# Kernel tuning notes

Measured on AMD Instinct MI355X. Metric: run time of the kernel, lower is better.

The kernel has to match this reference:

```python
import jax, jax.numpy as jnp
import numpy as np

TEMP = 0.05
MOMENTUM = 0.2
EPS = 1e-12

B, D, N = 64, 256, 200000


def setup_inputs() -> dict:
    key = jax.random.key(0)
    k1, k2, k3, k4 = jax.random.split(key, 4)
    inputs = jax.random.normal(k1, (B, D), dtype=jnp.float32)
    scores = jax.random.uniform(k2, (B,), dtype=jnp.float32)
    features = jax.random.normal(k3, (N, D), dtype=jnp.float32)
    # memory bank rows are kept L2-normalized by the update rule
    features = features / jnp.linalg.norm(features, axis=1, keepdims=True)
    targets = jax.random.randint(k4, (B,), 0, N, dtype=jnp.int64)
    return {"inputs": inputs, "scores": scores, "features": features, "targets": targets}


def reference(inputs, scores, features, targets):
    # L2-normalize query features (F.normalize(inputs, dim=1))
    x = inputs / jnp.maximum(jnp.linalg.norm(inputs, axis=1, keepdims=True), EPS)
    # memory-bank lookup: [B, N] logits against the full bank
    logits = jnp.einsum("bd,nd->bn", x, features) / TEMP
    logp = jax.nn.log_softmax(logits, axis=-1)
    per_sample_ce = -jnp.take_along_axis(logp, targets[:, None], axis=1)[:, 0]
    loss = jnp.sum(scores * per_sample_ce)
    # momentum scatter-update of the indexed bank rows with per-row renorm
    old = features[targets]                                   # [B, D] gather
    upd = MOMENTUM * old + (1.0 - MOMENTUM) * scores[:, None] * x
    upd = upd / jnp.maximum(jnp.linalg.norm(upd, axis=1, keepdims=True), EPS)
    new_features = features.at[targets].set(upd)
    return loss, new_features
```

## Files before the change

kernel.cpp:

```cpp
#include <hip/hip_runtime.h>
#include <hip/hip_bf16.h>

#define BB      64
#define DD      256
#define NROWS   200000
#define TEMP_INV 20.0f
#define MOM     0.2f
#define OMOM    0.8f
#define EPSN    1e-12f

#define TILE_R  16
#define NTILES  (NROWS / TILE_R)
#define GRID_B  1024

__device__ __forceinline__ float wave_allreduce_sum(float v) {
#pragma unroll
    for (int m = 32; m >= 1; m >>= 1) v += __shfl_xor(v, m, 64);
    return v;
}

__global__ void normalize_kernel(const float* __restrict__ inputs,
                                 float* __restrict__ xq,
                                 float* __restrict__ gsum,
                                 float* __restrict__ out) {
    int b = blockIdx.x, l = threadIdx.x;
    const float4* in4 = (const float4*)inputs;
    float4 v = in4[b * 64 + l];
    float ss = v.x * v.x + v.y * v.y + v.z * v.z + v.w * v.w;
    ss = wave_allreduce_sum(ss);
    float inv = 1.0f / fmaxf(sqrtf(ss), EPSN);
    float4 x = make_float4(v.x * inv, v.y * inv, v.z * inv, v.w * inv);
    ((float4*)xq)[l * 64 + b] = x;
    if (l == 0) gsum[b] = 0.0f;
    if (b == 0 && l == 0) out[0] = 0.0f;
}

__global__ __launch_bounds__(256, 3) void bank_kernel(
    const float* __restrict__ feat,
    const float* __restrict__ xq,
    float* __restrict__ out,
    float* __restrict__ gsum) {
    __shared__ float4 fld[TILE_R * 64];
    __shared__ float  part[4][TILE_R][BB];
    __shared__ float  fin[4][BB];

    int tid = threadIdx.x;
    int w = tid >> 6, l = tid & 63;

    const float4* xq4 = (const float4*)xq;
    float4 xr[16];
#pragma unroll
    for (int j = 0; j < 16; ++j) xr[j] = xq4[(w * 16 + j) * 64 + l];

    const float4* feat4 = (const float4*)feat;
    float* outF = out + 1;
    const float* fldF = (const float*)fld;
    float psum = 0.0f;

    for (int tile = blockIdx.x; tile < NTILES; tile += (int)gridDim.x) {
        int base4 = tile * (TILE_R * 64);
        float4 v0 = feat4[base4 + tid];
        float4 v1 = feat4[base4 + tid + 256];
        float4 v2 = feat4[base4 + tid + 512];
        float4 v3 = feat4[base4 + tid + 768];
        fld[tid]       = v0;
        fld[tid + 256] = v1;
        fld[tid + 512] = v2;
        fld[tid + 768] = v3;
        __syncthreads();

        int base = tile * (TILE_R * DD);
#pragma unroll
        for (int k = 0; k < 16; ++k)
            outF[base + tid + 256 * k] = fldF[tid + 256 * k];

        float p[TILE_R];
#pragma unroll
        for (int r = 0; r < TILE_R; ++r) p[r] = 0.0f;
#pragma unroll
        for (int j = 0; j < 16; ++j) {
            float4 xj = xr[j];
#pragma unroll
            for (int r = 0; r < TILE_R; ++r) {
                float4 f = fld[r * 64 + w * 16 + j];
                p[r] = fmaf(xj.x, f.x, p[r]);
                p[r] = fmaf(xj.y, f.y, p[r]);
                p[r] = fmaf(xj.z, f.z, p[r]);
                p[r] = fmaf(xj.w, f.w, p[r]);
            }
        }
#pragma unroll
        for (int r = 0; r < TILE_R; ++r) part[w][r][l] = p[r];
        __syncthreads();

#pragma unroll
        for (int i = 0; i < 4; ++i) {
            int r = (w << 2) | i;
            float dsum = part[0][r][l] + part[1][r][l]
                       + part[2][r][l] + part[3][r][l];
            psum += __expf(fmaf(dsum, TEMP_INV, -20.0f));
        }
        __syncthreads();
    }

    fin[w][l] = psum;
    __syncthreads();
    if (tid < BB) {
        float s = fin[0][tid] + fin[1][tid] + fin[2][tid] + fin[3][tid];
        atomicAdd(&gsum[tid], s);
    }
}

__global__ void update_kernel(const float* __restrict__ inputs,
                              const float* __restrict__ scores,
                              const float* __restrict__ feat,
                              const int* __restrict__ targets,
                              const float* __restrict__ gsum,
                              float* __restrict__ out) {
    int b = blockIdx.x, l = threadIdx.x;
    const float4* in4 = (const float4*)inputs;
    float4 v = in4[b * 64 + l];
    float ss = wave_allreduce_sum(v.x * v.x + v.y * v.y + v.z * v.z + v.w * v.w);
    float inv = 1.0f / fmaxf(sqrtf(ss), EPSN);
    float4 x = make_float4(v.x * inv, v.y * inv, v.z * inv, v.w * inv);

    int t = targets[b];
    const float4* feat4 = (const float4*)feat;
    float4 old = feat4[t * 64 + l];

    float dt = wave_allreduce_sum(x.x * old.x + x.y * old.y +
                                  x.z * old.z + x.w * old.w);
    float sc = scores[b];
    float c = OMOM * sc;
    float4 u = make_float4(MOM * old.x + c * x.x,
                           MOM * old.y + c * x.y,
                           MOM * old.z + c * x.z,
                           MOM * old.w + c * x.w);
    float us = wave_allreduce_sum(u.x * u.x + u.y * u.y + u.z * u.z + u.w * u.w);
    float uinv = 1.0f / fmaxf(sqrtf(us), EPSN);
    u.x *= uinv; u.y *= uinv; u.z *= uinv; u.w *= uinv;

    float* outF = out + 1;
    int bi = t * DD + 4 * l;
    outF[bi]     = u.x;
    outF[bi + 1] = u.y;
    outF[bi + 2] = u.z;
    outF[bi + 3] = u.w;

    if (l == 0) {
        float lse = 20.0f + logf(gsum[b]);
        float ce  = lse - dt * TEMP_INV;
        atomicAdd(&out[0], sc * ce);
    }
}

extern "C" void kernel_launch(void* const* d_in, const int* in_sizes, int n_in,
                              void* d_out, int out_size, void* d_ws, size_t ws_size,
                              hipStream_t stream) {
    const float* inputs  = (const float*)d_in[0];
    const float* scores  = (const float*)d_in[1];
    const float* feat    = (const float*)d_in[2];
    const int*   targets = (const int*)d_in[3];
    float* out = (float*)d_out;

    float* xq   = (float*)d_ws;
    float* gsum = xq + 16384;

    normalize_kernel<<<64, 64, 0, stream>>>(inputs, xq, gsum, out);
    bank_kernel<<<GRID_B, 256, 0, stream>>>(feat, xq, out, gsum);
    update_kernel<<<64, 64, 0, stream>>>(inputs, scores, feat, targets, gsum, out);
}
```

Baseline: 403.0 us.

## Compute bank logits with bf16 MFMA instead of fp32 FMA loops

Replaces the per-thread fp32 FMA dot products and the cross-wave shared-memory reduction with bf16 MFMA 16x16x32 instructions. The normalized queries are pre-packed into bf16 fragments, and each bank tile is converted to bf16 into a swizzled LDS buffer. Each wave owns 16 queries and accumulates the full K=256 itself, which removes the partial-sum array and one barrier per tile. Occupancy is raised via launch bounds. This lowers logit precision to bf16, which, with a temperature of 0.05 in the exponent, may shift the loss.

```diff
diff --git a/kernel.cpp b/kernel.cpp
--- a/kernel.cpp
+++ b/kernel.cpp
@@ -13,60 +13,94 @@
 #define NTILES  (NROWS / TILE_R)
 #define GRID_B  1024
 
+typedef __attribute__((ext_vector_type(8))) short  short8;
+typedef __attribute__((ext_vector_type(4))) float  f32x4;
+
 __device__ __forceinline__ float wave_allreduce_sum(float v) {
 #pragma unroll
     for (int m = 32; m >= 1; m >>= 1) v += __shfl_xor(v, m, 64);
     return v;
 }
 
+__device__ __forceinline__ ushort f2bf(float f) {
+    uint u = __float_as_uint(f);
+    u = (u + 0x7FFFu + ((u >> 16) & 1u)) >> 16;
+    return (ushort)u;
+}
+
 __global__ void normalize_kernel(const float* __restrict__ inputs,
-                                 float* __restrict__ xq,
+                                 uint4* __restrict__ xf,
                                  float* __restrict__ gsum,
                                  float* __restrict__ out) {
+    __shared__ float xs[DD];
     int b = blockIdx.x, l = threadIdx.x;
     const float4* in4 = (const float4*)inputs;
     float4 v = in4[b * 64 + l];
-    float ss = v.x * v.x + v.y * v.y + v.z * v.z + v.w * v.w;
-    ss = wave_allreduce_sum(ss);
+    float ss = wave_allreduce_sum(v.x * v.x + v.y * v.y + v.z * v.z + v.w * v.w);
     float inv = 1.0f / fmaxf(sqrtf(ss), EPSN);
-    float4 x = make_float4(v.x * inv, v.y * inv, v.z * inv, v.w * inv);
-    ((float4*)xq)[l * 64 + b] = x;
+    xs[4 * l + 0] = v.x * inv;
+    xs[4 * l + 1] = v.y * inv;
+    xs[4 * l + 2] = v.z * inv;
+    xs[4 * l + 3] = v.w * inv;
+    __syncthreads();
+    if (l < 32) {
+        int kc = l >> 2, g = l & 3;
+        int d0 = kc * 32 + g * 8;
+        ushort h[8];
+#pragma unroll
+        for (int j = 0; j < 8; ++j) h[j] = f2bf(xs[d0 + j]);
+        uint4 p;
+        p.x = (uint)h[0] | ((uint)h[1] << 16);
+        p.y = (uint)h[2] | ((uint)h[3] << 16);
+        p.z = (uint)h[4] | ((uint)h[5] << 16);
+        p.w = (uint)h[6] | ((uint)h[7] << 16);
+        xf[(b >> 4) * 512 + kc * 64 + g * 16 + (b & 15)] = p;
+    }
     if (l == 0) gsum[b] = 0.0f;
     if (b == 0 && l == 0) out[0] = 0.0f;
 }
 
-__global__ __launch_bounds__(256, 3) void bank_kernel(
+__global__ __launch_bounds__(256, 4) void bank_kernel(
     const float* __restrict__ feat,
-    const float* __restrict__ xq,
+    const uint4* __restrict__ xf,
     float* __restrict__ out,
     float* __restrict__ gsum) {
     __shared__ float4 fld[TILE_R * 64];
-    __shared__ float  part[4][TILE_R][BB];
-    __shared__ float  fin[4][BB];
+    __shared__ ushort bft[TILE_R * 256];
+    __shared__ float  fin[4][64][4];
 
     int tid = threadIdx.x;
     int w = tid >> 6, l = tid & 63;
+    int n16 = l & 15, g = l >> 4;
 
-    const float4* xq4 = (const float4*)xq;
-    float4 xr[16];
+    short8 afrag[8];
+    const short8* xf8 = (const short8*)xf;
 #pragma unroll
-    for (int j = 0; j < 16; ++j) xr[j] = xq4[(w * 16 + j) * 64 + l];
+    for (int kc = 0; kc < 8; ++kc) afrag[kc] = xf8[(w * 8 + kc) * 64 + l];
+
+    int boff[8];
+#pragma unroll
+    for (int kc = 0; kc < 8; ++kc)
+        boff[kc] = n16 * 512 + ((kc * 64 + g * 16) ^ ((n16 & 7) << 4));
 
     const float4* feat4 = (const float4*)feat;
     float* outF = out + 1;
     const float* fldF = (const float*)fld;
-    float psum = 0.0f;
+    float psum[4] = {0.f, 0.f, 0.f, 0.f};
 
     for (int tile = blockIdx.x; tile < NTILES; tile += (int)gridDim.x) {
         int base4 = tile * (TILE_R * 64);
-        float4 v0 = feat4[base4 + tid];
-        float4 v1 = feat4[base4 + tid + 256];
-        float4 v2 = feat4[base4 + tid + 512];
-        float4 v3 = feat4[base4 + tid + 768];
-        fld[tid]       = v0;
-        fld[tid + 256] = v1;
-        fld[tid + 512] = v2;
-        fld[tid + 768] = v3;
+#pragma unroll
+        for (int k = 0; k < 4; ++k) {
+            int flat = tid + 256 * k;
+            float4 v = feat4[base4 + flat];
+            fld[flat] = v;
+            int n = flat >> 6, c = flat & 63;
+            uint2 pk;
+            pk.x = (uint)f2bf(v.x) | ((uint)f2bf(v.y) << 16);
+            pk.y = (uint)f2bf(v.z) | ((uint)f2bf(v.w) << 16);
+            *(uint2*)((char*)bft + n * 512 + ((c * 8) ^ ((n & 7) << 4))) = pk;
+        }
         __syncthreads();
 
         int base = tile * (TILE_R * DD);
@@ -74,40 +108,27 @@
         for (int k = 0; k < 16; ++k)
             outF[base + tid + 256 * k] = fldF[tid + 256 * k];
 
-        float p[TILE_R];
+        f32x4 acc = {0.f, 0.f, 0.f, 0.f};
 #pragma unroll
-        for (int r = 0; r < TILE_R; ++r) p[r] = 0.0f;
-#pragma unroll
-        for (int j = 0; j < 16; ++j) {
-            float4 xj = xr[j];
-#pragma unroll
-            for (int r = 0; r < TILE_R; ++r) {
-                float4 f = fld[r * 64 + w * 16 + j];
-                p[r] = fmaf(xj.x, f.x, p[r]);
-                p[r] = fmaf(xj.y, f.y, p[r]);
-                p[r] = fmaf(xj.z, f.z, p[r]);
-                p[r] = fmaf(xj.w, f.w, p[r]);
-            }
+        for (int kc = 0; kc < 8; ++kc) {
+            short8 bfr = *(const short8*)((const char*)bft + boff[kc]);
+            acc = __builtin_amdgcn_mfma_f32_16x16x32_bf16(afrag[kc], bfr, acc, 0, 0, 0);
         }
 #pragma unroll
-        for (int r = 0; r < TILE_R; ++r) part[w][r][l] = p[r];
-        __syncthreads();
-
-#pragma unroll
-        for (int i = 0; i < 4; ++i) {
-            int r = (w << 2) | i;
-            float dsum = part[0][r][l] + part[1][r][l]
-                       + part[2][r][l] + part[3][r][l];
-            psum += __expf(fmaf(dsum, TEMP_INV, -20.0f));
-        }
+        for (int r = 0; r < 4; ++r)
+            psum[r] += __expf(fmaf(acc[r], TEMP_INV, -20.0f));
         __syncthreads();
     }
 
-    fin[w][l] = psum;
+#pragma unroll
+    for (int r = 0; r < 4; ++r) fin[w][l][r] = psum[r];
     __syncthreads();
     if (tid < BB) {
-        float s = fin[0][tid] + fin[1][tid] + fin[2][tid] + fin[3][tid];
-        atomicAdd(&gsum[tid], s);
+        int b = tid, bw = b >> 4, grp = (b >> 2) & 3, reg = b & 3;
+        float s = 0.f;
+#pragma unroll
+        for (int c = 0; c < 16; ++c) s += fin[bw][grp * 16 + c][reg];
+        atomicAdd(&gsum[b], s);
     }
 }
 
@@ -163,10 +184,10 @@
     const int*   targets = (const int*)d_in[3];
     float* out = (float*)d_out;
 
-    float* xq   = (float*)d_ws;
-    float* gsum = xq + 16384;
+    uint4* xf   = (uint4*)d_ws;
+    float* gsum = (float*)((char*)d_ws + 32768);
 
-    normalize_kernel<<<64, 64, 0, stream>>>(inputs, xq, gsum, out);
-    bank_kernel<<<GRID_B, 256, 0, stream>>>(feat, xq, out, gsum);
+    normalize_kernel<<<64, 64, 0, stream>>>(inputs, xf, gsum, out);
+    bank_kernel<<<GRID_B, 256, 0, stream>>>(feat, xf, out, gsum);
     update_kernel<<<64, 64, 0, stream>>>(inputs, scores, feat, targets, gsum, out);
 }
```

New measurement: 357.1 us. -11.4%, faster.
